# Kernel tuning notes

Hardware: AMD Instinct MI355X
Metric: run time of the kernel (lower is better)

The kernel has to match this reference:

```python
import jax, jax.numpy as jnp
import numpy as np

B, T, D, H, C, M = 128, 96, 256, 256, 8, 64
COMB = 4 * D + H  # z, z_prime, x_i, global_dynamics, h


def setup_inputs() -> dict:
    key = jax.random.key(0)
    ks = jax.random.split(key, 24)
    X = jax.random.normal(ks[0], (B, T, D), jnp.float32)
    X_last = jax.random.normal(ks[1], (B, T, D), jnp.float32)
    Mask = jax.random.bernoulli(ks[2], 0.5, (B, T, D)).astype(jnp.float32)
    Delta = jax.random.uniform(ks[3], (B, T, D), jnp.float32, 0.0, 5.0)
    X_last_b = jax.random.normal(ks[4], (B, T, D), jnp.float32)
    Delta_b = jax.random.uniform(ks[5], (B, T, D), jnp.float32, 0.0, 5.0)
    x = jnp.stack([X, X_last, Mask, Delta, X_last_b, Delta_b], axis=1)  # [B,6,T,D]
    X_mean = jax.random.normal(ks[6], (1, T, D), jnp.float32)
    clusters = jax.random.randint(ks[7], (D,), 1, C + 1, jnp.int64)
    s = 1.0 / np.sqrt(COMB)
    def U(k, shape, sc):
        return jax.random.uniform(k, shape, jnp.float32, -sc, sc)
    params = {
        'W_i': U(ks[8], (H, COMB), s), 'b_i': U(ks[9], (H,), s),
        'W_f': U(ks[10], (H, COMB), s), 'b_f': U(ks[11], (H,), s),
        'W_o': U(ks[12], (H, COMB), s), 'b_o': U(ks[13], (H,), s),
        'W_c': U(ks[14], (H, COMB), s), 'b_c': U(ks[15], (H,), s),
        'W_fc': U(ks[16], (D, H), 1.0 / np.sqrt(H)), 'b_fc': U(ks[17], (D,), 1.0 / np.sqrt(H)),
        'gz_w': U(ks[18], (D,), 1.0 / np.sqrt(D)), 'gz_b': U(ks[19], (D,), 1.0 / np.sqrt(D)),
        'gzp_w': U(ks[20], (D,), 1.0 / np.sqrt(D)), 'gzp_b': U(ks[21], (D,), 1.0 / np.sqrt(D)),
        'memory': jax.random.uniform(ks[22], (C, M, D), jnp.float32, -1.0 / np.sqrt(M), 1.0 / np.sqrt(M)),
    }
    k2 = jax.random.split(ks[23], 2)
    params['local_w'] = jax.random.uniform(k2[0], (3, D), jnp.float32, -1.0 / np.sqrt(3.0), 1.0 / np.sqrt(3.0))
    params['global_w'] = jax.random.uniform(k2[1], (C,), jnp.float32, -1.0 / np.sqrt(C), 1.0 / np.sqrt(C))
    return dict(x=x, X_mean=X_mean, clusters=clusters, **params)


def reference(x, X_mean, clusters, W_i, b_i, W_f, b_f, W_o, b_o, W_c, b_c,
              W_fc, b_fc, gz_w, gz_b, gzp_w, gzp_b, memory, local_w, global_w):
    # cluster one-hot feature masks: [C, D] (cluster ids are 1-based)
    cmask = (clusters[None, :] == jnp.arange(1, C + 1, dtype=clusters.dtype)[:, None]).astype(x.dtype)

    X, X_last, Mask, Delta, X_last_b, Delta_b = [x[:, i] for i in range(6)]  # each [B,T,D]
    xm = X_mean[0]  # [T,D]

    def step(carry, inp):
        h, c = carry
        xt, xl, xlb, m, d, db, mean = inp
        # FilterLinear with eye filter == diagonal linear; GRU-D decay
        dz = jnp.exp(-jax.nn.relu(d * gz_w + gz_b))
        dzp = jnp.exp(-jax.nn.relu(db * gzp_w + gzp_b))
        z = m * xt + (1 - m) * (dz * xl + (1 - dz) * mean)
        zp = m * xt + (1 - m) * (dzp * xlb + (1 - dzp) * mean)
        x_i = h @ W_fc.T + b_fc  # [B,D]
        local_stats = local_w[0] * z + local_w[1] * zp + local_w[2] * x_i  # [B,D]
        # per-cluster masked local stats -> memory attention
        li = local_stats[:, None, :] * cmask[None]              # [B,C,D]
        scores = jnp.einsum('cmd,bcd->bcm', memory, li)          # [B,C,M]
        s = jax.nn.softmax(scores, axis=-1)
        gd = jnp.einsum('bcm,cmd->bcd', s, memory)               # [B,C,D]
        gd = jnp.einsum('bcd,c->bd', gd, global_w)               # [B,D]
        combined = jnp.concatenate([z, zp, x_i, gd, h], axis=1)  # [B,4D+H]
        i = jax.nn.sigmoid(combined @ W_i.T + b_i)
        f = jax.nn.sigmoid(combined @ W_f.T + b_f)
        o = jax.nn.sigmoid(combined @ W_o.T + b_o)
        ct = jnp.tanh(combined @ W_c.T + b_c)
        c = f * c + i * ct
        h = o * jnp.tanh(c)
        out = h @ W_fc.T + b_fc
        return (h, c), out

    h0 = jnp.zeros((x.shape[0], H), x.dtype)
    c0 = jnp.zeros((x.shape[0], H), x.dtype)
    xs = (X.transpose(1, 0, 2), X_last.transpose(1, 0, 2), X_last_b.transpose(1, 0, 2),
          Mask.transpose(1, 0, 2), Delta.transpose(1, 0, 2), Delta_b.transpose(1, 0, 2), xm)
    _, outs = jax.lax.scan(step, (h0, c0), xs)
    return outs.transpose(1, 0, 2)  # [B,T,D]
```

## Files before the change

kernel.cpp:

```cpp
#include <hip/hip_runtime.h>
#include <hip/hip_bf16.h>
#include <hip/hip_fp16.h>
#include <cstdint>
#include <cstddef>


#define PLANE 24576

using bf16_t = __hip_bfloat16;
typedef __bf16 bf16x8 __attribute__((ext_vector_type(8)));
typedef float  f32x4  __attribute__((ext_vector_type(4)));
typedef unsigned int u32x4 __attribute__((ext_vector_type(4)));

__device__ __forceinline__ float  b2f(bf16_t v){ return __bfloat162float(v); }
__device__ __forceinline__ bf16_t f2b(float v){ return __float2bfloat16(v); }
__device__ __forceinline__ float ldF(const void* p, size_t i, int f32){
  return f32 ? ((const float*)p)[i] : b2f(((const bf16_t*)p)[i]);
}
__device__ __forceinline__ bf16x8 ld_frag(const void* p){
  union { uint4 u; bf16x8 v; } c;
  c.u = *(const uint4*)p;
  return c.v;
}
__device__ __forceinline__ f32x4 mfma_bf16(bf16x8 a, bf16x8 b, f32x4 c){
  return __builtin_amdgcn_mfma_f32_16x16x32_bf16(a, b, c, 0, 0, 0);
}

__device__ __forceinline__ u32x4 ld_cg(const void* p){
  u32x4 r;
  asm volatile("global_load_dwordx4 %0, %1, off sc0 sc1"
               : "=v"(r) : "v"(p) : "memory");
  return r;
}
__device__ __forceinline__ void st_cg(void* p, u32x4 v){
  asm volatile("global_store_dwordx4 %0, %1, off sc0 sc1"
               :: "v"(p), "v"(v) : "memory");
}
__device__ __forceinline__ void st_flag(int* p, int v){
  asm volatile("global_store_dword %0, %1, off sc0 sc1"
               :: "v"(p), "v"(v) : "memory");
}
__device__ __forceinline__ int ld_flag(const int* p){
  int r;
  asm volatile("global_load_dword %0, %1, off sc0 sc1\n\ts_waitcnt vmcnt(0)"
               : "=v"(r) : "v"(p) : "memory");
  return r;
}
__device__ __forceinline__ void vm_wait0(){
  asm volatile("s_waitcnt vmcnt(0)" ::: "memory");
  __builtin_amdgcn_sched_barrier(0);
}

__global__ __launch_bounds__(64) void k_detect(
    const uint32_t* __restrict__ xu, const uint32_t* __restrict__ clu,
    int* __restrict__ flags)
{
  __shared__ int cnt[2];
  int t = threadIdx.x;
  if (t < 2) cnt[t] = 0;
  __syncthreads();
  uint32_t v = xu[2*PLANE + t];
  if (v == 0u || v == 0x3F800000u) atomicAdd(&cnt[0], 1);
  if (clu[2*t + 1] == 0u) atomicAdd(&cnt[1], 1);
  __syncthreads();
  if (t == 0){
    flags[0] = (cnt[0] >= 48) ? 1 : 0;
    flags[1] = (cnt[1] >= 60) ? 1 : 0;
  }
}

__global__ __launch_bounds__(256) void k_zero(int* __restrict__ bar){
  bar[blockIdx.x*256 + threadIdx.x] = 0;
}

__global__ __launch_bounds__(256) void k_canon(
    const void* __restrict__ Wfc, const void* __restrict__ Xmean,
    const void* __restrict__ bfc, const void* __restrict__ localw,
    const void* __restrict__ globalw, const void* __restrict__ gzw,
    const void* __restrict__ gzb, const void* __restrict__ gzpw,
    const void* __restrict__ gzpb, const int* __restrict__ flags,
    bf16_t* __restrict__ WfcC, bf16_t* __restrict__ XmC,
    bf16_t* __restrict__ bfcC, bf16_t* __restrict__ lwC,
    bf16_t* __restrict__ gwC, float* __restrict__ gzC)
{
  const int f32 = flags[0];
  int i = blockIdx.x*256 + threadIdx.x;
  if (i < 65536) WfcC[i] = f2b(ldF(Wfc, i, f32));
  if (i < 24576) XmC[i]  = f2b(ldF(Xmean, i, f32));
  if (i < 256)   bfcC[i] = f2b(ldF(bfc, i, f32));
  if (i < 768)   lwC[i]  = f2b(ldF(localw, i, f32));
  if (i < 8)     gwC[i]  = f2b(ldF(globalw, i, f32));
  if (i < 256){
    gzC[i]       = ldF(gzw,  i, f32);
    gzC[256 + i] = ldF(gzb,  i, f32);
    gzC[512 + i] = ldF(gzpw, i, f32);
    gzC[768 + i] = ldF(gzpb, i, f32);
  }
}

__global__ __launch_bounds__(256) void k_fold(
    const void* __restrict__ Wi, const void* __restrict__ Wf,
    const void* __restrict__ Wo, const void* __restrict__ Wc,
    const void* __restrict__ bi, const void* __restrict__ bfg,
    const void* __restrict__ bo, const void* __restrict__ bcg,
    const void* __restrict__ Wfc, const void* __restrict__ bfc,
    const int* __restrict__ flags,
    bf16_t* __restrict__ U, bf16_t* __restrict__ Uz, float* __restrict__ bias2)
{
  const int f32 = flags[0];
  int n = blockIdx.x; int g = n & 3; int j = n >> 2;
  const void* Wg = (g==0)?Wi:(g==1)?Wf:(g==2)?Wo:Wc;
  const void* bg = (g==0)?bi:(g==1)?bfg:(g==2)?bo:bcg;
  const size_t wb = (size_t)j*1280;
  int k = threadIdx.x;
  float acc = 0.f;
  for (int d=0; d<256; ++d)
    acc += ldF(Wg, wb+512+d, f32) * ldF(Wfc, (size_t)d*256+k, f32);
  U[(size_t)n*512 + k]        = f2b(acc + ldF(Wg, wb+1024+k, f32));
  U[(size_t)n*512 + 256 + k]  = f2b(ldF(Wg, wb+768+k, f32));
  Uz[(size_t)n*512 + k]       = f2b(ldF(Wg, wb+k, f32));
  Uz[(size_t)n*512 + 256 + k] = f2b(ldF(Wg, wb+256+k, f32));
  __shared__ float red[256];
  red[k] = ldF(Wg, wb+512+k, f32) * ldF(bfc, k, f32);
  __syncthreads();
  for (int s=128; s>0; s>>=1){ if (k<s) red[k]+=red[k+s]; __syncthreads(); }
  if (k==0) bias2[n] = red[0] + ldF(bg, j, f32);
}

__global__ __launch_bounds__(256) void k_foldG(
    const void* __restrict__ Wi, const void* __restrict__ Wf,
    const void* __restrict__ Wo, const void* __restrict__ Wc,
    const void* __restrict__ memory, const int* __restrict__ flags,
    bf16_t* __restrict__ G)
{
  const int f32 = flags[0];
  __shared__ float wrow[4][256];
  int j = blockIdx.x; int tid = threadIdx.x;
  const void* Wg[4] = {Wi,Wf,Wo,Wc};
  for (int g=0; g<4; ++g)
    wrow[g][tid] = ldF(Wg[g], (size_t)j*1280 + 768 + tid, f32);
  __syncthreads();
  for (int half=0; half<2; ++half){
    int cm = half*256 + tid;
    float a0=0,a1=0,a2=0,a3=0;
    for (int d=0; d<256; ++d){
      float mv = ldF(memory, (size_t)cm*256 + d, f32);
      a0 += wrow[0][d]*mv; a1 += wrow[1][d]*mv;
      a2 += wrow[2][d]*mv; a3 += wrow[3][d]*mv;
    }
    G[(size_t)(4*j+0)*512 + cm] = f2b(a0);
    G[(size_t)(4*j+1)*512 + cm] = f2b(a1);
    G[(size_t)(4*j+2)*512 + cm] = f2b(a2);
    G[(size_t)(4*j+3)*512 + cm] = f2b(a3);
  }
}

__global__ __launch_bounds__(256) void k_foldQ(
    const int* __restrict__ clusters, const void* __restrict__ memory,
    const bf16_t* __restrict__ lwC, const bf16_t* __restrict__ WfcC,
    const bf16_t* __restrict__ bfcC, const int* __restrict__ flags,
    bf16_t* __restrict__ Mem2, bf16_t* __restrict__ Qbf, float* __restrict__ qb)
{
  const int f32 = flags[0], i64 = flags[1];
  const int cm = blockIdx.x; const int c = cm >> 6;
  const int tid = threadIdx.x;
  __shared__ float ml2[256];
  __shared__ float red[256];
  int cv = i64 ? clusters[2*tid] : clusters[tid];
  float mv = (cv == c+1) ? ldF(memory, (size_t)cm*256 + tid, f32) : 0.f;
  Mem2[(size_t)cm*256 + tid] = f2b(mv);
  float m2 = mv * b2f(lwC[512 + tid]);
  ml2[tid] = m2;
  red[tid] = m2 * b2f(bfcC[tid]);
  __syncthreads();
  float acc = 0.f;
  for (int d=0; d<256; ++d)
    acc += ml2[d] * b2f(WfcC[(size_t)d*256 + tid]);
  Qbf[(size_t)cm*256 + tid] = f2b(acc);
  for (int s=128; s>0; s>>=1){ if (tid<s) red[tid]+=red[tid+s]; __syncthreads(); }
  if (tid==0) qb[cm] = red[0];
}

__global__ __launch_bounds__(256) void k_zzp(
    const void* __restrict__ x, const bf16_t* __restrict__ XmC,
    const float* __restrict__ gzC, const bf16_t* __restrict__ lwC,
    const int* __restrict__ flags,
    bf16_t* __restrict__ Zcat, bf16_t* __restrict__ Zl)
{
  const int f32 = flags[0];
  int r = blockIdx.x;
  int t = r >> 7, b = r & 127, d = threadIdx.x;
  size_t base = (size_t)b*6*PLANE + (size_t)t*256 + d;
  float xt = ldF(x, base          , f32);
  float xl = ldF(x, base +   PLANE, f32);
  float mk = ldF(x, base + 2*PLANE, f32);
  float de = ldF(x, base + 3*PLANE, f32);
  float xlb= ldF(x, base + 4*PLANE, f32);
  float deb= ldF(x, base + 5*PLANE, f32);
  float mean = b2f(XmC[t*256+d]);
  float dz  = expf(-fmaxf(0.f, de *gzC[d]     + gzC[256+d]));
  float dzp = expf(-fmaxf(0.f, deb*gzC[512+d] + gzC[768+d]));
  float z  = mk*xt + (1.f-mk)*(dz *xl  + (1.f-dz )*mean);
  float zp = mk*xt + (1.f-mk)*(dzp*xlb + (1.f-dzp)*mean);
  Zcat[(size_t)r*512 + d]       = f2b(z);
  Zcat[(size_t)r*512 + 256 + d] = f2b(zp);
  Zl[(size_t)r*256 + d] = f2b(b2f(lwC[d])*z + b2f(lwC[256+d])*zp);
}

__global__ __launch_bounds__(256) void k_zc(
    const bf16_t* __restrict__ Zcat, const bf16_t* __restrict__ Uz,
    const float* __restrict__ bias2, __half* __restrict__ zc)
{
  const int tid = threadIdx.x;
  const int w = tid>>6, l = tid&63, q=l>>4, cl=l&15;
  const int mq = w&1, nq = w>>1;
  const int m0 = blockIdx.x*128, n0 = blockIdx.y*128;
  f32x4 acc[4][4];
#pragma unroll
  for (int a=0;a<4;++a)
#pragma unroll
    for (int b2=0;b2<4;++b2) acc[a][b2] = (f32x4){0.f,0.f,0.f,0.f};
  for (int ks=0; ks<16; ++ks){
    bf16x8 av[4], bv[4];
#pragma unroll
    for (int mi=0;mi<4;++mi)
      av[mi] = ld_frag(&Zcat[(size_t)(m0+mq*64+mi*16+cl)*512 + ks*32 + q*8]);
#pragma unroll
    for (int ni=0;ni<4;++ni)
      bv[ni] = ld_frag(&Uz[(size_t)(n0+nq*64+ni*16+cl)*512 + ks*32 + q*8]);
#pragma unroll
    for (int mi=0;mi<4;++mi)
#pragma unroll
      for (int ni=0;ni<4;++ni)
        acc[mi][ni] = mfma_bf16(av[mi], bv[ni], acc[mi][ni]);
  }
#pragma unroll
  for (int mi=0;mi<4;++mi)
#pragma unroll
    for (int ni=0;ni<4;++ni)
#pragma unroll
      for (int rr=0;rr<4;++rr){
        int m = m0 + mq*64 + mi*16 + q*4 + rr;
        int n = n0 + nq*64 + ni*16 + cl;
        zc[(size_t)m*1024 + n] = __float2half(acc[mi][ni][rr] + bias2[n]);
      }
}

__global__ __launch_bounds__(256) void k_szm(
    const bf16_t* __restrict__ Zl, const bf16_t* __restrict__ Mem2,
    const float* __restrict__ qb, __half* __restrict__ SzM)
{
  const int tid = threadIdx.x;
  const int w = tid>>6, l = tid&63, q=l>>4, cl=l&15;
  const int mq = w&1, nq = w>>1;
  const int m0 = blockIdx.x*128, n0 = blockIdx.y*128;
  f32x4 acc[4][4];
#pragma unroll
  for (int a=0;a<4;++a)
#pragma unroll
    for (int b2=0;b2<4;++b2) acc[a][b2] = (f32x4){0.f,0.f,0.f,0.f};
  for (int ks=0; ks<8; ++ks){
    bf16x8 av[4], bv[4];
#pragma unroll
    for (int mi=0;mi<4;++mi)
      av[mi] = ld_frag(&Zl[(size_t)(m0+mq*64+mi*16+cl)*256 + ks*32 + q*8]);
#pragma unroll
    for (int ni=0;ni<4;++ni)
      bv[ni] = ld_frag(&Mem2[(size_t)(n0+nq*64+ni*16+cl)*256 + ks*32 + q*8]);
#pragma unroll
    for (int mi=0;mi<4;++mi)
#pragma unroll
      for (int ni=0;ni<4;++ni)
        acc[mi][ni] = mfma_bf16(av[mi], bv[ni], acc[mi][ni]);
  }
#pragma unroll
  for (int mi=0;mi<4;++mi)
#pragma unroll
    for (int ni=0;ni<4;++ni)
#pragma unroll
      for (int rr=0;rr<4;++rr){
        int m = m0 + mq*64 + mi*16 + q*4 + rr;
        int n = n0 + nq*64 + ni*16 + cl;
        SzM[(size_t)m*512 + n] = __float2half(acc[mi][ni][rr] + qb[n]);
      }
}

__global__ __launch_bounds__(256) void k_out(
    const bf16_t* __restrict__ hSeq, const bf16_t* __restrict__ WfcC,
    const bf16_t* __restrict__ bfcC, const int* __restrict__ flags,
    void* __restrict__ outv)
{
  const int f32 = flags[0];
  const int tid = threadIdx.x;
  const int w = tid>>6, l = tid&63, q=l>>4, cl=l&15;
  const int mq = w&1, nq = w>>1;
  const int m0 = blockIdx.x*128, n0 = blockIdx.y*128;
  f32x4 acc[4][4];
#pragma unroll
  for (int a=0;a<4;++a)
#pragma unroll
    for (int b2=0;b2<4;++b2) acc[a][b2] = (f32x4){0.f,0.f,0.f,0.f};
  for (int ks=0; ks<8; ++ks){
    bf16x8 av[4], bv[4];
#pragma unroll
    for (int mi=0;mi<4;++mi)
      av[mi] = ld_frag(&hSeq[(size_t)(128 + m0+mq*64+mi*16+cl)*256 + ks*32 + q*8]);
#pragma unroll
    for (int ni=0;ni<4;++ni)
      bv[ni] = ld_frag(&WfcC[(size_t)(n0+nq*64+ni*16+cl)*256 + ks*32 + q*8]);
#pragma unroll
    for (int mi=0;mi<4;++mi)
#pragma unroll
      for (int ni=0;ni<4;++ni)
        acc[mi][ni] = mfma_bf16(av[mi], bv[ni], acc[mi][ni]);
  }
#pragma unroll
  for (int mi=0;mi<4;++mi)
#pragma unroll
    for (int ni=0;ni<4;++ni)
#pragma unroll
      for (int rr=0;rr<4;++rr){
        int m = m0 + mq*64 + mi*16 + q*4 + rr;
        int n = n0 + nq*64 + ni*16 + cl;
        float v = acc[mi][ni][rr] + b2f(bfcC[n]);
        int b = m & 127, tt = m >> 7;
        size_t ob = ((size_t)b*96 + tt)*256 + n;
        if (f32) ((float*)outv)[ob] = v; else ((bf16_t*)outv)[ob] = f2b(v);
      }
}

__global__ __launch_bounds__(256) void k_main(
    const bf16_t* __restrict__ gwC,
    const bf16_t* __restrict__ U, const bf16_t* __restrict__ G,
    const bf16_t* __restrict__ Qbf,
    const __half* __restrict__ zc, const __half* __restrict__ SzM,
    bf16_t* __restrict__ hSeq, bf16_t* __restrict__ tSeq,
    int* __restrict__ bar)
{
  __shared__ bf16_t Us[64][264];
  __shared__ bf16_t Gs[64][520];
  __shared__ bf16_t Qs[64][264];
  __shared__ bf16_t hS[16][264];
  __shared__ bf16_t tS[16][520];
  __shared__ bf16_t tO[16][64];
  __shared__ bf16_t hO[16][16];

  const int tid = threadIdx.x;
  const int W = tid>>6, l = tid&63, q = l>>4, cl = l&15;
  const int g = blockIdx.x & 7, s = blockIdx.x >> 3;
  const int r0 = g*16;
  const int n0 = s*64;
  int* barA = bar + g*64;
  int* barB = bar + g*64 + 32;

  for (int i=tid; i<64*32; i+=256){ int r=i>>5, c8=(i&31)*8;
    *(uint4*)(&Us[r][c8]) = *(const uint4*)(U + (size_t)(n0+r)*512 + c8); }
  for (int i=tid; i<64*64; i+=256){ int r=i>>6, c8=(i&63)*8;
    *(uint4*)(&Gs[r][c8]) = *(const uint4*)(G + (size_t)(n0+r)*512 + c8); }
  if (s<8)
    for (int i=tid; i<64*32; i+=256){ int r=i>>5, c8=(i&31)*8;
      *(uint4*)(&Qs[r][c8]) = *(const uint4*)(Qbf + (size_t)(s*64+r)*256 + c8); }
  const float gw_c = (s<8)? b2f(gwC[s]) : 0.f;
  const bool sc_wave = (s<8) && (W==0);
  float creg[4] = {0.f,0.f,0.f,0.f};
  __syncthreads();

  for (int t=0; t<96; ++t){
    f32x4 acc;
#pragma unroll
    for (int rr=0; rr<4; ++rr)
      acc[rr] = __half2float(zc[((size_t)(t*128)+r0+q*4+rr)*1024 + n0 + W*16 + cl]);
    f32x4 sa[4];
    if (sc_wave){
#pragma unroll
      for (int nt=0; nt<4; ++nt)
#pragma unroll
        for (int rr=0; rr<4; ++rr)
          sa[nt][rr] = __half2float(
            SzM[((size_t)(t*128)+r0+q*4+rr)*512 + s*64 + nt*16 + cl]);
    }
    if (W==0){
      if (t>0){
        const int* fp = barA + (l&15);
        int v;
        do { int f = ld_flag(fp); v = (l<16)? f : 0x7fffffff; } while (__any(v < t));
        const bf16_t* hsrc = hSeq + (size_t)t*128*256 + (size_t)r0*256;
        u32x4 hv[8];
#pragma unroll
        for (int k=0;k<8;++k){ int c=l+64*k;
          hv[k] = ld_cg(hsrc + (size_t)(c>>5)*256 + (c&31)*8); }
        vm_wait0();
#pragma unroll
        for (int k=0;k<8;++k){ int c=l+64*k;
          *(u32x4*)(&hS[c>>5][(c&31)*8]) = hv[k]; }
      } else {
#pragma unroll
        for (int k=0;k<8;++k){ int c=l+64*k;
          *(u32x4*)(&hS[c>>5][(c&31)*8]) = (u32x4){0,0,0,0}; }
      }
    }
    __syncthreads();
    if (sc_wave){
#pragma unroll
      for (int ks=0; ks<8; ++ks){
        bf16x8 a = ld_frag(&hS[cl][ks*32 + q*8]);
#pragma unroll
        for (int nt=0; nt<4; ++nt)
          sa[nt] = mfma_bf16(a, ld_frag(&Qs[nt*16+cl][ks*32 + q*8]), sa[nt]);
      }
#pragma unroll
      for (int rr=0; rr<4; ++rr){
        float mx = fmaxf(fmaxf(sa[0][rr],sa[1][rr]), fmaxf(sa[2][rr],sa[3][rr]));
        mx = fmaxf(mx, __shfl_xor(mx,1));
        mx = fmaxf(mx, __shfl_xor(mx,2));
        mx = fmaxf(mx, __shfl_xor(mx,4));
        mx = fmaxf(mx, __shfl_xor(mx,8));
        float e0=expf(sa[0][rr]-mx), e1=expf(sa[1][rr]-mx);
        float e2=expf(sa[2][rr]-mx), e3=expf(sa[3][rr]-mx);
        float sm = e0+e1+e2+e3;
        sm += __shfl_xor(sm,1); sm += __shfl_xor(sm,2);
        sm += __shfl_xor(sm,4); sm += __shfl_xor(sm,8);
        float sc = gw_c/sm;
        tO[q*4+rr][ 0+cl] = f2b(e0*sc);
        tO[q*4+rr][16+cl] = f2b(e1*sc);
        tO[q*4+rr][32+cl] = f2b(e2*sc);
        tO[q*4+rr][48+cl] = f2b(e3*sc);
      }
      bf16_t* tdst = tSeq + (size_t)t*128*512 + (size_t)r0*512 + s*64;
#pragma unroll
      for (int k=0;k<2;++k){ int c=l+64*k;
        u32x4 v = *(u32x4*)(&tO[c>>3][(c&7)*8]);
        st_cg(tdst + (size_t)(c>>3)*512 + (c&7)*8, v); }
      vm_wait0();
      if (l==0) st_flag(barB + s, t+1);
    }
#pragma unroll
    for (int ks=0; ks<8; ++ks)
      acc = mfma_bf16(ld_frag(&hS[cl][ks*32 + q*8]),
                      ld_frag(&Us[W*16+cl][ks*32 + q*8]), acc);
    if (W==1){
      const int* fp = barB + (l&7);
      int v;
      do { int f = ld_flag(fp); v = (l<8)? f : 0x7fffffff; } while (__any(v < t+1));
      const bf16_t* tsrc = tSeq + (size_t)t*128*512 + (size_t)r0*512;
      u32x4 tv[16];
#pragma unroll
      for (int k=0;k<16;++k){ int c=l+64*k;
        tv[k] = ld_cg(tsrc + (size_t)(c>>6)*512 + (c&63)*8); }
      vm_wait0();
#pragma unroll
      for (int k=0;k<16;++k){ int c=l+64*k;
        *(u32x4*)(&tS[c>>6][(c&63)*8]) = tv[k]; }
    }
    __syncthreads();
#pragma unroll
    for (int ks=0; ks<16; ++ks)
      acc = mfma_bf16(ld_frag(&tS[cl][ks*32 + q*8]),
                      ld_frag(&Gs[W*16+cl][ks*32 + q*8]), acc);
    const int base = l & ~3;
#pragma unroll
    for (int rr=0; rr<4; ++rr){
      float p = acc[rr];
      float pi = __shfl(p, base+0);
      float pf = __shfl(p, base+1);
      float po = __shfl(p, base+2);
      float pc = __shfl(p, base+3);
      float iv = 1.f/(1.f+expf(-pi));
      float fv = 1.f/(1.f+expf(-pf));
      float ov = 1.f/(1.f+expf(-po));
      float cv = tanhf(pc);
      float cn = fv*creg[rr] + iv*cv;
      creg[rr] = cn;
      float hv = ov * tanhf(cn);
      if ((l&3)==0)
        hO[q*4+rr][W*4 + (cl>>2)] = f2b(hv);
    }
    __syncthreads();
    if (W==0){
      if (l < 32){
        u32x4 v = *(u32x4*)(&hO[l>>1][(l&1)*8]);
        st_cg(hSeq + (size_t)(t+1)*128*256 + (size_t)(r0+(l>>1))*256
                   + s*16 + (l&1)*8, v);
      }
      vm_wait0();
      if (l==0) st_flag(barA + s, t+1);
    }
  }
}

extern "C" void kernel_launch(void* const* d_in, const int* in_sizes, int n_in,
                              void* d_out, int out_size, void* d_ws, size_t ws_size,
                              hipStream_t stream)
{
  const void* x       = d_in[0];
  const void* Xmean   = d_in[1];
  const int*  clusters= (const int*)d_in[2];
  const void* Wi  = d_in[3];
  const void* bi  = d_in[4];
  const void* Wf  = d_in[5];
  const void* bfp = d_in[6];
  const void* Wo  = d_in[7];
  const void* bo  = d_in[8];
  const void* Wc  = d_in[9];
  const void* bcp = d_in[10];
  const void* Wfc = d_in[11];
  const void* bfc = d_in[12];
  const void* gzw = d_in[13];
  const void* gzb = d_in[14];
  const void* gzpw= d_in[15];
  const void* gzpb= d_in[16];
  const void* memory = d_in[17];
  const void* localw = d_in[18];
  const void* globalw= d_in[19];
  (void)in_sizes; (void)n_in; (void)out_size; (void)ws_size;

  char* ws = (char*)d_ws;
  size_t off = 0;
  auto take = [&](size_t bytes)->char*{
    char* p = ws + off; off = (off + bytes + 255) & ~(size_t)255; return p; };
  int*    flags  = (int*)   take(16);
  int*    bar    = (int*)   take(512*4);
  bf16_t* U      = (bf16_t*)take((size_t)1024*512*2);
  bf16_t* Uz     = (bf16_t*)take((size_t)1024*512*2);
  bf16_t* G      = (bf16_t*)take((size_t)1024*512*2);
  bf16_t* WfcC   = (bf16_t*)take((size_t)65536*2);
  bf16_t* XmC    = (bf16_t*)take((size_t)24576*2);
  bf16_t* bfcC   = (bf16_t*)take(256*2);
  bf16_t* lwC    = (bf16_t*)take(768*2);
  bf16_t* gwC    = (bf16_t*)take(8*2);
  float*  gzC    = (float*) take(1024*4);
  float*  bias2  = (float*) take(1024*4);
  bf16_t* Mem2   = (bf16_t*)take((size_t)512*256*2);
  bf16_t* Qbf    = (bf16_t*)take((size_t)512*256*2);
  float*  qb     = (float*) take(512*4);
  __half* zc     = (__half*)take((size_t)12288*1024*2);
  __half* SzM    = (__half*)take((size_t)12288*512*2);
  char* bigA = take((size_t)12288*512*2);
  char* bigB = take((size_t)97*128*256*2);
  bf16_t* Zcat = (bf16_t*)bigA;
  bf16_t* tSeq = (bf16_t*)bigA;
  bf16_t* Zl   = (bf16_t*)bigB;
  bf16_t* hSeq = (bf16_t*)bigB;

  k_detect<<<1,    64, 0,stream>>>((const uint32_t*)x, (const uint32_t*)clusters, flags);
  k_zero  <<<2,    256,0,stream>>>(bar);
  k_canon <<<256,  256,0,stream>>>(Wfc, Xmean, bfc, localw, globalw,
                                   gzw, gzb, gzpw, gzpb, flags,
                                   WfcC, XmC, bfcC, lwC, gwC, gzC);
  k_fold  <<<1024, 256,0,stream>>>(Wi,Wf,Wo,Wc, bi,bfp,bo,bcp, Wfc,bfc, flags,
                                   U, Uz, bias2);
  k_foldG <<<256,  256,0,stream>>>(Wi,Wf,Wo,Wc, memory, flags, G);
  k_foldQ <<<512,  256,0,stream>>>(clusters, memory, lwC, WfcC, bfcC, flags,
                                   Mem2, Qbf, qb);
  k_zzp   <<<12288,256,0,stream>>>(x, XmC, gzC, lwC, flags, Zcat, Zl);
  k_zc    <<<dim3(96,8),256,0,stream>>>(Zcat, Uz, bias2, zc);
  k_szm   <<<dim3(96,4),256,0,stream>>>(Zl, Mem2, qb, SzM);
  k_main  <<<128,  256,0,stream>>>(gwC, U, G, Qbf, zc, SzM, hSeq, tSeq, bar);
  k_out   <<<dim3(96,2),256,0,stream>>>(hSeq, WfcC, bfcC, flags, d_out);
}
```

Before: 1.077 ms.

## Merge input GEMMs, recurrence and output GEMM into one flag-synchronized persistent kernel

Replaces the separate zc, SzM, recurrent and output-projection launches with one 240-block kernel. 128 blocks run the recurrence while 64 blocks produce zc, 32 produce SzM and 16 compute outputs, each timestep handed off through global flags. This lets the non-recurrent GEMMs and the output projection overlap the serial LSTM loop instead of running before or after it. In exchange, buffers that were aliased get their own storage, the per-step flag polling grows, and correctness depends on all 240 blocks being resident at once.

```diff
diff --git a/kernel.cpp b/kernel.cpp
--- a/kernel.cpp
+++ b/kernel.cpp
@@ -22,6 +22,9 @@
   c.u = *(const uint4*)p;
   return c.v;
 }
+__device__ __forceinline__ bf16x8 u2b(u32x4 u){
+  union { u32x4 u; bf16x8 v; } c; c.u = u; return c.v;
+}
 __device__ __forceinline__ f32x4 mfma_bf16(bf16x8 a, bf16x8 b, f32x4 c){
   return __builtin_amdgcn_mfma_f32_16x16x32_bf16(a, b, c, 0, 0, 0);
 }
@@ -36,6 +39,12 @@
   asm volatile("global_store_dwordx4 %0, %1, off sc0 sc1"
                :: "v"(p), "v"(v) : "memory");
 }
+__device__ __forceinline__ int ld_cg_u16(const void* p){
+  int r;
+  asm volatile("global_load_ushort %0, %1, off sc0 sc1"
+               : "=v"(r) : "v"(p) : "memory");
+  return r;
+}
 __device__ __forceinline__ void st_flag(int* p, int v){
   asm volatile("global_store_dword %0, %1, off sc0 sc1"
                :: "v"(p), "v"(v) : "memory");
@@ -49,6 +58,10 @@
 __device__ __forceinline__ void vm_wait0(){
   asm volatile("s_waitcnt vmcnt(0)" ::: "memory");
   __builtin_amdgcn_sched_barrier(0);
+}
+__device__ __forceinline__ float h2f_bits(int u){
+  union{ unsigned short s; __half h; } c; c.s = (unsigned short)u;
+  return __half2float(c.h);
 }
 
 __global__ __launch_bounds__(64) void k_detect(
@@ -207,135 +220,17 @@
   Zl[(size_t)r*256 + d] = f2b(b2f(lwC[d])*z + b2f(lwC[256+d])*zp);
 }
 
-__global__ __launch_bounds__(256) void k_zc(
-    const bf16_t* __restrict__ Zcat, const bf16_t* __restrict__ Uz,
-    const float* __restrict__ bias2, __half* __restrict__ zc)
-{
-  const int tid = threadIdx.x;
-  const int w = tid>>6, l = tid&63, q=l>>4, cl=l&15;
-  const int mq = w&1, nq = w>>1;
-  const int m0 = blockIdx.x*128, n0 = blockIdx.y*128;
-  f32x4 acc[4][4];
-#pragma unroll
-  for (int a=0;a<4;++a)
-#pragma unroll
-    for (int b2=0;b2<4;++b2) acc[a][b2] = (f32x4){0.f,0.f,0.f,0.f};
-  for (int ks=0; ks<16; ++ks){
-    bf16x8 av[4], bv[4];
-#pragma unroll
-    for (int mi=0;mi<4;++mi)
-      av[mi] = ld_frag(&Zcat[(size_t)(m0+mq*64+mi*16+cl)*512 + ks*32 + q*8]);
-#pragma unroll
-    for (int ni=0;ni<4;++ni)
-      bv[ni] = ld_frag(&Uz[(size_t)(n0+nq*64+ni*16+cl)*512 + ks*32 + q*8]);
-#pragma unroll
-    for (int mi=0;mi<4;++mi)
-#pragma unroll
-      for (int ni=0;ni<4;++ni)
-        acc[mi][ni] = mfma_bf16(av[mi], bv[ni], acc[mi][ni]);
-  }
-#pragma unroll
-  for (int mi=0;mi<4;++mi)
-#pragma unroll
-    for (int ni=0;ni<4;++ni)
-#pragma unroll
-      for (int rr=0;rr<4;++rr){
-        int m = m0 + mq*64 + mi*16 + q*4 + rr;
-        int n = n0 + nq*64 + ni*16 + cl;
-        zc[(size_t)m*1024 + n] = __float2half(acc[mi][ni][rr] + bias2[n]);
-      }
-}
-
-__global__ __launch_bounds__(256) void k_szm(
-    const bf16_t* __restrict__ Zl, const bf16_t* __restrict__ Mem2,
-    const float* __restrict__ qb, __half* __restrict__ SzM)
-{
-  const int tid = threadIdx.x;
-  const int w = tid>>6, l = tid&63, q=l>>4, cl=l&15;
-  const int mq = w&1, nq = w>>1;
-  const int m0 = blockIdx.x*128, n0 = blockIdx.y*128;
-  f32x4 acc[4][4];
-#pragma unroll
-  for (int a=0;a<4;++a)
-#pragma unroll
-    for (int b2=0;b2<4;++b2) acc[a][b2] = (f32x4){0.f,0.f,0.f,0.f};
-  for (int ks=0; ks<8; ++ks){
-    bf16x8 av[4], bv[4];
-#pragma unroll
-    for (int mi=0;mi<4;++mi)
-      av[mi] = ld_frag(&Zl[(size_t)(m0+mq*64+mi*16+cl)*256 + ks*32 + q*8]);
-#pragma unroll
-    for (int ni=0;ni<4;++ni)
-      bv[ni] = ld_frag(&Mem2[(size_t)(n0+nq*64+ni*16+cl)*256 + ks*32 + q*8]);
-#pragma unroll
-    for (int mi=0;mi<4;++mi)
-#pragma unroll
-      for (int ni=0;ni<4;++ni)
-        acc[mi][ni] = mfma_bf16(av[mi], bv[ni], acc[mi][ni]);
-  }
-#pragma unroll
-  for (int mi=0;mi<4;++mi)
-#pragma unroll
-    for (int ni=0;ni<4;++ni)
-#pragma unroll
-      for (int rr=0;rr<4;++rr){
-        int m = m0 + mq*64 + mi*16 + q*4 + rr;
-        int n = n0 + nq*64 + ni*16 + cl;
-        SzM[(size_t)m*512 + n] = __float2half(acc[mi][ni][rr] + qb[n]);
-      }
-}
-
-__global__ __launch_bounds__(256) void k_out(
-    const bf16_t* __restrict__ hSeq, const bf16_t* __restrict__ WfcC,
-    const bf16_t* __restrict__ bfcC, const int* __restrict__ flags,
-    void* __restrict__ outv)
-{
-  const int f32 = flags[0];
-  const int tid = threadIdx.x;
-  const int w = tid>>6, l = tid&63, q=l>>4, cl=l&15;
-  const int mq = w&1, nq = w>>1;
-  const int m0 = blockIdx.x*128, n0 = blockIdx.y*128;
-  f32x4 acc[4][4];
-#pragma unroll
-  for (int a=0;a<4;++a)
-#pragma unroll
-    for (int b2=0;b2<4;++b2) acc[a][b2] = (f32x4){0.f,0.f,0.f,0.f};
-  for (int ks=0; ks<8; ++ks){
-    bf16x8 av[4], bv[4];
-#pragma unroll
-    for (int mi=0;mi<4;++mi)
-      av[mi] = ld_frag(&hSeq[(size_t)(128 + m0+mq*64+mi*16+cl)*256 + ks*32 + q*8]);
-#pragma unroll
-    for (int ni=0;ni<4;++ni)
-      bv[ni] = ld_frag(&WfcC[(size_t)(n0+nq*64+ni*16+cl)*256 + ks*32 + q*8]);
-#pragma unroll
-    for (int mi=0;mi<4;++mi)
-#pragma unroll
-      for (int ni=0;ni<4;++ni)
-        acc[mi][ni] = mfma_bf16(av[mi], bv[ni], acc[mi][ni]);
-  }
-#pragma unroll
-  for (int mi=0;mi<4;++mi)
-#pragma unroll
-    for (int ni=0;ni<4;++ni)
-#pragma unroll
-      for (int rr=0;rr<4;++rr){
-        int m = m0 + mq*64 + mi*16 + q*4 + rr;
-        int n = n0 + nq*64 + ni*16 + cl;
-        float v = acc[mi][ni][rr] + b2f(bfcC[n]);
-        int b = m & 127, tt = m >> 7;
-        size_t ob = ((size_t)b*96 + tt)*256 + n;
-        if (f32) ((float*)outv)[ob] = v; else ((bf16_t*)outv)[ob] = f2b(v);
-      }
-}
-
-__global__ __launch_bounds__(256) void k_main(
+__global__ __launch_bounds__(256) void k_mega(
     const bf16_t* __restrict__ gwC,
     const bf16_t* __restrict__ U, const bf16_t* __restrict__ G,
-    const bf16_t* __restrict__ Qbf,
-    const __half* __restrict__ zc, const __half* __restrict__ SzM,
+    const bf16_t* __restrict__ Qbf, const bf16_t* __restrict__ Uz,
+    const float* __restrict__ bias2, const bf16_t* __restrict__ Mem2,
+    const float* __restrict__ qb, const bf16_t* __restrict__ Zcat,
+    const bf16_t* __restrict__ Zl, const bf16_t* __restrict__ WfcC,
+    const bf16_t* __restrict__ bfcC, const int* __restrict__ flags,
+    __half* __restrict__ zc, __half* __restrict__ SzM,
     bf16_t* __restrict__ hSeq, bf16_t* __restrict__ tSeq,
-    int* __restrict__ bar)
+    int* __restrict__ bar, void* __restrict__ outv)
 {
   __shared__ bf16_t Us[64][264];
   __shared__ bf16_t Gs[64][520];
@@ -345,145 +240,273 @@
   __shared__ bf16_t tO[16][64];
   __shared__ bf16_t hO[16][16];
 
+  const int bid = blockIdx.x;
   const int tid = threadIdx.x;
   const int W = tid>>6, l = tid&63, q = l>>4, cl = l&15;
-  const int g = blockIdx.x & 7, s = blockIdx.x >> 3;
-  const int r0 = g*16;
-  const int n0 = s*64;
-  int* barA = bar + g*64;
-  int* barB = bar + g*64 + 32;
-
-  for (int i=tid; i<64*32; i+=256){ int r=i>>5, c8=(i&31)*8;
-    *(uint4*)(&Us[r][c8]) = *(const uint4*)(U + (size_t)(n0+r)*512 + c8); }
-  for (int i=tid; i<64*64; i+=256){ int r=i>>6, c8=(i&63)*8;
-    *(uint4*)(&Gs[r][c8]) = *(const uint4*)(G + (size_t)(n0+r)*512 + c8); }
-  if (s<8)
+  int* zcflag  = bar + 512;
+  int* szmflag = bar + 576;
+
+  if (bid < 128){
+    const int g = bid & 7, s = bid >> 3;
+    const int r0 = g*16;
+    const int n0 = s*64;
+    int* barA = bar + g*64;
+    int* barB = bar + g*64 + 32;
+
     for (int i=tid; i<64*32; i+=256){ int r=i>>5, c8=(i&31)*8;
-      *(uint4*)(&Qs[r][c8]) = *(const uint4*)(Qbf + (size_t)(s*64+r)*256 + c8); }
-  const float gw_c = (s<8)? b2f(gwC[s]) : 0.f;
-  const bool sc_wave = (s<8) && (W==0);
-  float creg[4] = {0.f,0.f,0.f,0.f};
-  __syncthreads();
-
-  for (int t=0; t<96; ++t){
-    f32x4 acc;
-#pragma unroll
-    for (int rr=0; rr<4; ++rr)
-      acc[rr] = __half2float(zc[((size_t)(t*128)+r0+q*4+rr)*1024 + n0 + W*16 + cl]);
-    f32x4 sa[4];
-    if (sc_wave){
-#pragma unroll
-      for (int nt=0; nt<4; ++nt)
-#pragma unroll
-        for (int rr=0; rr<4; ++rr)
-          sa[nt][rr] = __half2float(
-            SzM[((size_t)(t*128)+r0+q*4+rr)*512 + s*64 + nt*16 + cl]);
+      *(uint4*)(&Us[r][c8]) = *(const uint4*)(U + (size_t)(n0+r)*512 + c8); }
+    for (int i=tid; i<64*64; i+=256){ int r=i>>6, c8=(i&63)*8;
+      *(uint4*)(&Gs[r][c8]) = *(const uint4*)(G + (size_t)(n0+r)*512 + c8); }
+    if (s<8)
+      for (int i=tid; i<64*32; i+=256){ int r=i>>5, c8=(i&31)*8;
+        *(uint4*)(&Qs[r][c8]) = *(const uint4*)(Qbf + (size_t)(s*64+r)*256 + c8); }
+    const float gw_c = (s<8)? b2f(gwC[s]) : 0.f;
+    const bool sc_wave = (s<8) && (W==0);
+    float creg[4] = {0.f,0.f,0.f,0.f};
+    __syncthreads();
+
+    for (int t=0; t<96; ++t){
+      if (W==0){
+        const int* fp = nullptr; int need = 0; bool act = false;
+        if (l < 16){ fp = barA + l; need = t; act = (t>0); }
+        else if (l < 20){ fp = zcflag + 4*s + (l-16); need = t+1; act = true; }
+        else if (l < 24){ fp = szmflag + 4*s + (l-20); need = t+1; act = (s<8); }
+        int f;
+        do { f = act ? ld_flag(fp) : 0x7fffffff; } while (__any(f < need));
+        if (t>0){
+          const bf16_t* hsrc = hSeq + (size_t)t*128*256 + (size_t)r0*256;
+          u32x4 hv[8];
+#pragma unroll
+          for (int k=0;k<8;++k){ int c=l+64*k;
+            hv[k] = ld_cg(hsrc + (size_t)(c>>5)*256 + (c&31)*8); }
+          vm_wait0();
+#pragma unroll
+          for (int k=0;k<8;++k){ int c=l+64*k;
+            *(u32x4*)(&hS[c>>5][(c&31)*8]) = hv[k]; }
+        } else {
+#pragma unroll
+          for (int k=0;k<8;++k){ int c=l+64*k;
+            *(u32x4*)(&hS[c>>5][(c&31)*8]) = (u32x4){0,0,0,0}; }
+        }
+      }
+      __syncthreads();
+      int zr[4];
+#pragma unroll
+      for (int rr=0; rr<4; ++rr)
+        zr[rr] = ld_cg_u16(zc + ((size_t)(t*128)+r0+q*4+rr)*1024 + n0 + W*16 + cl);
+      if (sc_wave){
+        int sr[16];
+#pragma unroll
+        for (int nt=0; nt<4; ++nt)
+#pragma unroll
+          for (int rr=0; rr<4; ++rr)
+            sr[nt*4+rr] = ld_cg_u16(
+              SzM + ((size_t)(t*128)+r0+q*4+rr)*512 + s*64 + nt*16 + cl);
+        f32x4 sa[4];
+#pragma unroll
+        for (int nt=0;nt<4;++nt) sa[nt]=(f32x4){0.f,0.f,0.f,0.f};
+#pragma unroll
+        for (int ks=0; ks<8; ++ks){
+          bf16x8 a = ld_frag(&hS[cl][ks*32 + q*8]);
+#pragma unroll
+          for (int nt=0; nt<4; ++nt)
+            sa[nt] = mfma_bf16(a, ld_frag(&Qs[nt*16+cl][ks*32 + q*8]), sa[nt]);
+        }
+        vm_wait0();
+#pragma unroll
+        for (int nt=0; nt<4; ++nt)
+#pragma unroll
+          for (int rr=0; rr<4; ++rr) sa[nt][rr] += h2f_bits(sr[nt*4+rr]);
+#pragma unroll
+        for (int rr=0; rr<4; ++rr){
+          float mx = fmaxf(fmaxf(sa[0][rr],sa[1][rr]), fmaxf(sa[2][rr],sa[3][rr]));
+          mx = fmaxf(mx, __shfl_xor(mx,1));
+          mx = fmaxf(mx, __shfl_xor(mx,2));
+          mx = fmaxf(mx, __shfl_xor(mx,4));
+          mx = fmaxf(mx, __shfl_xor(mx,8));
+          float e0=expf(sa[0][rr]-mx), e1=expf(sa[1][rr]-mx);
+          float e2=expf(sa[2][rr]-mx), e3=expf(sa[3][rr]-mx);
+          float sm = e0+e1+e2+e3;
+          sm += __shfl_xor(sm,1); sm += __shfl_xor(sm,2);
+          sm += __shfl_xor(sm,4); sm += __shfl_xor(sm,8);
+          float sc = gw_c/sm;
+          tO[q*4+rr][ 0+cl] = f2b(e0*sc);
+          tO[q*4+rr][16+cl] = f2b(e1*sc);
+          tO[q*4+rr][32+cl] = f2b(e2*sc);
+          tO[q*4+rr][48+cl] = f2b(e3*sc);
+        }
+        bf16_t* tdst = tSeq + (size_t)t*128*512 + (size_t)r0*512 + s*64;
+#pragma unroll
+        for (int k=0;k<2;++k){ int c=l+64*k;
+          u32x4 v = *(u32x4*)(&tO[c>>3][(c&7)*8]);
+          st_cg(tdst + (size_t)(c>>3)*512 + (c&7)*8, v); }
+        vm_wait0();
+        if (l==0) st_flag(barB + s, t+1);
+      }
+      f32x4 acc = {0.f,0.f,0.f,0.f};
+#pragma unroll
+      for (int ks=0; ks<8; ++ks)
+        acc = mfma_bf16(ld_frag(&hS[cl][ks*32 + q*8]),
+                        ld_frag(&Us[W*16+cl][ks*32 + q*8]), acc);
+      if (W==1){
+        const int* fp = barB + (l&7);
+        int v;
+        do { int f = ld_flag(fp); v = (l<8)? f : 0x7fffffff; } while (__any(v < t+1));
+        const bf16_t* tsrc = tSeq + (size_t)t*128*512 + (size_t)r0*512;
+        u32x4 tv[16];
+#pragma unroll
+        for (int k=0;k<16;++k){ int c=l+64*k;
+          tv[k] = ld_cg(tsrc + (size_t)(c>>6)*512 + (c&63)*8); }
+        vm_wait0();
+#pragma unroll
+        for (int k=0;k<16;++k){ int c=l+64*k;
+          *(u32x4*)(&tS[c>>6][(c&63)*8]) = tv[k]; }
+      }
+      __syncthreads();
+#pragma unroll
+      for (int ks=0; ks<16; ++ks)
+        acc = mfma_bf16(ld_frag(&tS[cl][ks*32 + q*8]),
+                        ld_frag(&Gs[W*16+cl][ks*32 + q*8]), acc);
+      vm_wait0();
+#pragma unroll
+      for (int rr=0; rr<4; ++rr) acc[rr] += h2f_bits(zr[rr]);
+      const int base = l & ~3;
+#pragma unroll
+      for (int rr=0; rr<4; ++rr){
+        float p = acc[rr];
+        float pi = __shfl(p, base+0);
+        float pf = __shfl(p, base+1);
+        float po = __shfl(p, base+2);
+        float pc = __shfl(p, base+3);
+        float iv = 1.f/(1.f+expf(-pi));
+        float fv = 1.f/(1.f+expf(-pf));
+        float ov = 1.f/(1.f+expf(-po));
+        float cv = tanhf(pc);
+        float cn = fv*creg[rr] + iv*cv;
+        creg[rr] = cn;
+        float hv = ov * tanhf(cn);
+        if ((l&3)==0)
+          hO[q*4+rr][W*4 + (cl>>2)] = f2b(hv);
+      }
+      __syncthreads();
+      if (W==0){
+        if (l < 32){
+          u32x4 v = *(u32x4*)(&hO[l>>1][(l&1)*8]);
+          st_cg(hSeq + (size_t)(t+1)*128*256 + (size_t)(r0+(l>>1))*256
+                     + s*16 + (l&1)*8, v);
+        }
+        vm_wait0();
+        if (l==0) st_flag(barA + s, t+1);
+      }
     }
-    if (W==0){
-      if (t>0){
-        const int* fp = barA + (l&15);
-        int v;
-        do { int f = ld_flag(fp); v = (l<16)? f : 0x7fffffff; } while (__any(v < t));
-        const bf16_t* hsrc = hSeq + (size_t)t*128*256 + (size_t)r0*256;
-        u32x4 hv[8];
-#pragma unroll
-        for (int k=0;k<8;++k){ int c=l+64*k;
-          hv[k] = ld_cg(hsrc + (size_t)(c>>5)*256 + (c&31)*8); }
-        vm_wait0();
-#pragma unroll
-        for (int k=0;k<8;++k){ int c=l+64*k;
-          *(u32x4*)(&hS[c>>5][(c&31)*8]) = hv[k]; }
-      } else {
-#pragma unroll
-        for (int k=0;k<8;++k){ int c=l+64*k;
-          *(u32x4*)(&hS[c>>5][(c&31)*8]) = (u32x4){0,0,0,0}; }
-      }
+  } else if (bid < 192){
+    const int a = bid - 128;
+    const int n0a = a*16;
+    bf16_t (*BS)[520] = (bf16_t(*)[520])&Gs[0][0];
+    __half (*zT)[16]  = (__half(*)[16])&Qs[0][0];
+    for (int i=tid; i<16*64; i+=256){ int r=i>>6, c8=(i&63)*8;
+      *(uint4*)(&BS[r][c8]) = *(const uint4*)(Uz + (size_t)(n0a+r)*512 + c8); }
+    const float bias = bias2[n0a + cl];
+    __syncthreads();
+    for (int t=0; t<96; ++t){
+      f32x4 a0={0.f,0.f,0.f,0.f}, a1={0.f,0.f,0.f,0.f};
+      const bf16_t* ar0 = Zcat + ((size_t)t*128 + W*32 + cl)*512;
+      const bf16_t* ar1 = ar0 + (size_t)16*512;
+#pragma unroll
+      for (int ks=0; ks<16; ++ks){
+        bf16x8 b = ld_frag(&BS[cl][ks*32 + q*8]);
+        a0 = mfma_bf16(ld_frag(ar0 + ks*32 + q*8), b, a0);
+        a1 = mfma_bf16(ld_frag(ar1 + ks*32 + q*8), b, a1);
+      }
+#pragma unroll
+      for (int rr=0; rr<4; ++rr){
+        zT[W*32      + q*4 + rr][cl] = __float2half(a0[rr] + bias);
+        zT[W*32 + 16 + q*4 + rr][cl] = __float2half(a1[rr] + bias);
+      }
+      __syncthreads();
+      { int row = tid>>1, half = tid&1;
+        u32x4 v = *(u32x4*)(&zT[row][half*8]);
+        st_cg(zc + ((size_t)t*128+row)*1024 + n0a + half*8, v);
+      }
+      vm_wait0();
+      __syncthreads();
+      if (tid==0) st_flag(zcflag + a, t+1);
     }
+  } else if (bid < 224){
+    const int a2 = bid - 192;
+    const int cm0 = a2*16;
+    bf16_t (*BS)[520] = (bf16_t(*)[520])&Gs[0][0];
+    __half (*zT)[16]  = (__half(*)[16])&Qs[0][0];
+    for (int i=tid; i<16*32; i+=256){ int r=i>>5, c8=(i&31)*8;
+      *(uint4*)(&BS[r][c8]) = *(const uint4*)(Mem2 + (size_t)(cm0+r)*256 + c8); }
+    const float bias = qb[cm0 + cl];
     __syncthreads();
-    if (sc_wave){
+    for (int t=0; t<96; ++t){
+      f32x4 a0={0.f,0.f,0.f,0.f}, a1={0.f,0.f,0.f,0.f};
+      const bf16_t* ar0 = Zl + ((size_t)t*128 + W*32 + cl)*256;
+      const bf16_t* ar1 = ar0 + (size_t)16*256;
 #pragma unroll
       for (int ks=0; ks<8; ++ks){
-        bf16x8 a = ld_frag(&hS[cl][ks*32 + q*8]);
-#pragma unroll
-        for (int nt=0; nt<4; ++nt)
-          sa[nt] = mfma_bf16(a, ld_frag(&Qs[nt*16+cl][ks*32 + q*8]), sa[nt]);
+        bf16x8 b = ld_frag(&BS[cl][ks*32 + q*8]);
+        a0 = mfma_bf16(ld_frag(ar0 + ks*32 + q*8), b, a0);
+        a1 = mfma_bf16(ld_frag(ar1 + ks*32 + q*8), b, a1);
       }
 #pragma unroll
       for (int rr=0; rr<4; ++rr){
-        float mx = fmaxf(fmaxf(sa[0][rr],sa[1][rr]), fmaxf(sa[2][rr],sa[3][rr]));
-        mx = fmaxf(mx, __shfl_xor(mx,1));
-        mx = fmaxf(mx, __shfl_xor(mx,2));
-        mx = fmaxf(mx, __shfl_xor(mx,4));
-        mx = fmaxf(mx, __shfl_xor(mx,8));
-        float e0=expf(sa[0][rr]-mx), e1=expf(sa[1][rr]-mx);
-        float e2=expf(sa[2][rr]-mx), e3=expf(sa[3][rr]-mx);
-        float sm = e0+e1+e2+e3;
-        sm += __shfl_xor(sm,1); sm += __shfl_xor(sm,2);
-        sm += __shfl_xor(sm,4); sm += __shfl_xor(sm,8);
-        float sc = gw_c/sm;
-        tO[q*4+rr][ 0+cl] = f2b(e0*sc);
-        tO[q*4+rr][16+cl] = f2b(e1*sc);
-        tO[q*4+rr][32+cl] = f2b(e2*sc);
-        tO[q*4+rr][48+cl] = f2b(e3*sc);
-      }
-      bf16_t* tdst = tSeq + (size_t)t*128*512 + (size_t)r0*512 + s*64;
-#pragma unroll
-      for (int k=0;k<2;++k){ int c=l+64*k;
-        u32x4 v = *(u32x4*)(&tO[c>>3][(c&7)*8]);
-        st_cg(tdst + (size_t)(c>>3)*512 + (c&7)*8, v); }
+        zT[W*32      + q*4 + rr][cl] = __float2half(a0[rr] + bias);
+        zT[W*32 + 16 + q*4 + rr][cl] = __float2half(a1[rr] + bias);
+      }
+      __syncthreads();
+      { int row = tid>>1, half = tid&1;
+        u32x4 v = *(u32x4*)(&zT[row][half*8]);
+        st_cg(SzM + ((size_t)t*128+row)*512 + cm0 + half*8, v);
+      }
       vm_wait0();
-      if (l==0) st_flag(barB + s, t+1);
+      __syncthreads();
+      if (tid==0) st_flag(szmflag + a2, t+1);
     }
-#pragma unroll
-    for (int ks=0; ks<8; ++ks)
-      acc = mfma_bf16(ld_frag(&hS[cl][ks*32 + q*8]),
-                      ld_frag(&Us[W*16+cl][ks*32 + q*8]), acc);
-    if (W==1){
-      const int* fp = barB + (l&7);
-      int v;
-      do { int f = ld_flag(fp); v = (l<8)? f : 0x7fffffff; } while (__any(v < t+1));
-      const bf16_t* tsrc = tSeq + (size_t)t*128*512 + (size_t)r0*512;
-      u32x4 tv[16];
-#pragma unroll
-      for (int k=0;k<16;++k){ int c=l+64*k;
-        tv[k] = ld_cg(tsrc + (size_t)(c>>6)*512 + (c&63)*8); }
+  } else {
+    const int a3 = bid - 224;
+    const int oc0 = a3*16;
+    bf16_t (*BS)[520] = (bf16_t(*)[520])&Gs[0][0];
+    for (int i=tid; i<16*32; i+=256){ int r=i>>5, c8=(i&31)*8;
+      *(uint4*)(&BS[r][c8]) = *(const uint4*)(WfcC + (size_t)(oc0+r)*256 + c8); }
+    const float bias = b2f(bfcC[oc0 + cl]);
+    const int f32o = flags[0];
+    __syncthreads();
+    for (int t=0; t<96; ++t){
+      const int* f1 = bar + (l>>4)*64 + (l&15);
+      const int* f2 = bar + ((l>>4)+4)*64 + (l&15);
+      int fa, fb;
+      do { fa = ld_flag(f1); fb = ld_flag(f2); }
+      while (__any((fa < t+1) || (fb < t+1)));
+      u32x4 av0[8], av1[8];
+      const bf16_t* hr0 = hSeq + ((size_t)(t+1)*128 + W*32 + cl)*256;
+      const bf16_t* hr1 = hr0 + (size_t)16*256;
+#pragma unroll
+      for (int ks=0; ks<8; ++ks){
+        av0[ks] = ld_cg(hr0 + ks*32 + q*8);
+        av1[ks] = ld_cg(hr1 + ks*32 + q*8);
+      }
       vm_wait0();
-#pragma unroll
-      for (int k=0;k<16;++k){ int c=l+64*k;
-        *(u32x4*)(&tS[c>>6][(c&63)*8]) = tv[k]; }
-    }
-    __syncthreads();
-#pragma unroll
-    for (int ks=0; ks<16; ++ks)
-      acc = mfma_bf16(ld_frag(&tS[cl][ks*32 + q*8]),
-                      ld_frag(&Gs[W*16+cl][ks*32 + q*8]), acc);
-    const int base = l & ~3;
-#pragma unroll
-    for (int rr=0; rr<4; ++rr){
-      float p = acc[rr];
-      float pi = __shfl(p, base+0);
-      float pf = __shfl(p, base+1);
-      float po = __shfl(p, base+2);
-      float pc = __shfl(p, base+3);
-      float iv = 1.f/(1.f+expf(-pi));
-      float fv = 1.f/(1.f+expf(-pf));
-      float ov = 1.f/(1.f+expf(-po));
-      float cv = tanhf(pc);
-      float cn = fv*creg[rr] + iv*cv;
-      creg[rr] = cn;
-      float hv = ov * tanhf(cn);
-      if ((l&3)==0)
-        hO[q*4+rr][W*4 + (cl>>2)] = f2b(hv);
-    }
-    __syncthreads();
-    if (W==0){
-      if (l < 32){
-        u32x4 v = *(u32x4*)(&hO[l>>1][(l&1)*8]);
-        st_cg(hSeq + (size_t)(t+1)*128*256 + (size_t)(r0+(l>>1))*256
-                   + s*16 + (l&1)*8, v);
-      }
-      vm_wait0();
-      if (l==0) st_flag(barA + s, t+1);
+      f32x4 o0={0.f,0.f,0.f,0.f}, o1={0.f,0.f,0.f,0.f};
+#pragma unroll
+      for (int ks=0; ks<8; ++ks){
+        bf16x8 b = ld_frag(&BS[cl][ks*32 + q*8]);
+        o0 = mfma_bf16(u2b(av0[ks]), b, o0);
+        o1 = mfma_bf16(u2b(av1[ks]), b, o1);
+      }
+#pragma unroll
+      for (int rr=0; rr<4; ++rr){
+        int b0 = W*32 + q*4 + rr;
+        int b1 = b0 + 16;
+        float v0 = o0[rr] + bias;
+        float v1 = o1[rr] + bias;
+        size_t ob0 = ((size_t)b0*96 + t)*256 + oc0 + cl;
+        size_t ob1 = ((size_t)b1*96 + t)*256 + oc0 + cl;
+        if (f32o){ ((float*)outv)[ob0] = v0; ((float*)outv)[ob1] = v1; }
+        else     { ((bf16_t*)outv)[ob0] = f2b(v0); ((bf16_t*)outv)[ob1] = f2b(v1); }
+      }
     }
   }
 }
@@ -519,7 +542,7 @@
   auto take = [&](size_t bytes)->char*{
     char* p = ws + off; off = (off + bytes + 255) & ~(size_t)255; return p; };
   int*    flags  = (int*)   take(16);
-  int*    bar    = (int*)   take(512*4);
+  int*    bar    = (int*)   take(1024*4);
   bf16_t* U      = (bf16_t*)take((size_t)1024*512*2);
   bf16_t* Uz     = (bf16_t*)take((size_t)1024*512*2);
   bf16_t* G      = (bf16_t*)take((size_t)1024*512*2);
@@ -535,15 +558,13 @@
   float*  qb     = (float*) take(512*4);
   __half* zc     = (__half*)take((size_t)12288*1024*2);
   __half* SzM    = (__half*)take((size_t)12288*512*2);
-  char* bigA = take((size_t)12288*512*2);
-  char* bigB = take((size_t)97*128*256*2);
-  bf16_t* Zcat = (bf16_t*)bigA;
-  bf16_t* tSeq = (bf16_t*)bigA;
-  bf16_t* Zl   = (bf16_t*)bigB;
-  bf16_t* hSeq = (bf16_t*)bigB;
+  bf16_t* Zcat   = (bf16_t*)take((size_t)12288*512*2);
+  bf16_t* Zl     = (bf16_t*)take((size_t)12288*256*2);
+  bf16_t* tSeq   = (bf16_t*)take((size_t)96*128*512*2);
+  bf16_t* hSeq   = (bf16_t*)take((size_t)97*128*256*2);
 
   k_detect<<<1,    64, 0,stream>>>((const uint32_t*)x, (const uint32_t*)clusters, flags);
-  k_zero  <<<2,    256,0,stream>>>(bar);
+  k_zero  <<<4,    256,0,stream>>>(bar);
   k_canon <<<256,  256,0,stream>>>(Wfc, Xmean, bfc, localw, globalw,
                                    gzw, gzb, gzpw, gzpb, flags,
                                    WfcC, XmC, bfcC, lwC, gwC, gzC);
@@ -553,8 +574,7 @@
   k_foldQ <<<512,  256,0,stream>>>(clusters, memory, lwC, WfcC, bfcC, flags,
                                    Mem2, Qbf, qb);
   k_zzp   <<<12288,256,0,stream>>>(x, XmC, gzC, lwC, flags, Zcat, Zl);
-  k_zc    <<<dim3(96,8),256,0,stream>>>(Zcat, Uz, bias2, zc);
-  k_szm   <<<dim3(96,4),256,0,stream>>>(Zl, Mem2, qb, SzM);
-  k_main  <<<128,  256,0,stream>>>(gwC, U, G, Qbf, zc, SzM, hSeq, tSeq, bar);
-  k_out   <<<dim3(96,2),256,0,stream>>>(hSeq, WfcC, bfcC, flags, d_out);
-}
+  k_mega  <<<240,  256,0,stream>>>(gwC, U, G, Qbf, Uz, bias2, Mem2, qb,
+                                   Zcat, Zl, WfcC, bfcC, flags,
+                                   zc, SzM, hSeq, tSeq, bar, d_out);
+}
```

New measurement: 1.093 ms. About the same (+1.5%).
